# Kernel tuning notes

Hardware: AMD Instinct MI355X
Metric: run time of the kernel (lower is better)

## Reference

```python
import jax, jax.numpy as jnp
import numpy as np

B, N = 512, 128
K = 3                      # top-k per row/col
CONF_THRESH = 0.05
ACCEPT_RADIUS = 0.1
CORR_THRESHOLD = 3         # min correspondences per patch
CORR_LIMIT = 2048          # verification-set size (correspondence_limit)
NUM_REFINE = 5
EPS = 1e-5


def setup_inputs() -> dict:
    key = jax.random.key(0)
    k1, k2, k3, k4, k5 = jax.random.split(key, 5)
    return {
        'score_mat': jax.random.normal(k1, (B, N, N), dtype=jnp.float32),
        'ref_knn_points': jax.random.normal(k2, (B, N, 3), dtype=jnp.float32),
        'src_knn_points': jax.random.normal(k3, (B, N, 3), dtype=jnp.float32),
        'ref_knn_masks': jax.random.bernoulli(k4, 0.95, (B, N)),
        'src_knn_masks': jax.random.bernoulli(k5, 0.95, (B, N)),
    }


def _svd_transform(H, src_c, ref_c):
    """H: (..., 3, 3) covariance; src_c/ref_c: (..., 3) centroids -> (..., 4, 4)."""
    U, _, Vh = jnp.linalg.svd(H)
    V = jnp.swapaxes(Vh, -1, -2)
    Ut = jnp.swapaxes(U, -1, -2)
    d = jnp.sign(jnp.linalg.det(V @ Ut))
    E = jnp.zeros_like(H).at[..., 0, 0].set(1.0).at[..., 1, 1].set(1.0).at[..., 2, 2].set(d)
    R = V @ E @ Ut
    t = ref_c - jnp.einsum('...ij,...j->...i', R, src_c)
    T = jnp.zeros(H.shape[:-2] + (4, 4), H.dtype)
    T = T.at[..., :3, :3].set(R).at[..., :3, 3].set(t).at[..., 3, 3].set(1.0)
    return T


def weighted_procrustes(src, ref, w):
    """src/ref: (C, 3), w: (C,) -> (4, 4). weight_thresh=0, weights >= 0 so no clamp."""
    wn = w / (jnp.sum(w, axis=-1, keepdims=True) + EPS)
    sc = jnp.einsum('n,nc->c', wn, src)
    rc = jnp.einsum('n,nc->c', wn, ref)
    H = jnp.einsum('nc,n,nd->cd', src - sc, wn, ref - rc)
    return _svd_transform(H, sc, rc)


def _topk_mask_last(scores):
    """Keep top-K values along the last axis of (B, R, S), zeros elsewhere."""
    vals, idx = jax.lax.top_k(scores, K)
    b = jnp.arange(scores.shape[0])[:, None, None]
    r = jnp.arange(scores.shape[1])[None, :, None]
    return jnp.zeros_like(scores).at[b, r, idx].set(vals)


def reference(score_mat, ref_knn_points, src_knn_points, ref_knn_masks, src_knn_masks):
    scores = jnp.exp(score_mat)  # score_mat holds log-scores (GeoTransformer forward)

    # --- correspondence matrix: dual top-k scatter + mutual + valid masks ---
    ref_corr = _topk_mask_last(scores) > CONF_THRESH
    src_corr = jnp.swapaxes(_topk_mask_last(jnp.swapaxes(scores, 1, 2)), 1, 2) > CONF_THRESH
    corr = ref_corr & src_corr  # mutual=True
    corr = corr & (ref_knn_masks[:, :, None] & src_knn_masks[:, None, :])

    masked = scores * corr.astype(scores.dtype)  # (B, N, N)
    patch_count = jnp.sum(corr, axis=(1, 2))      # correspondences per patch

    # --- per-patch weighted procrustes over all (n, m) pairs, zero-weighted pads ---
    wn = masked / (jnp.sum(masked, axis=(1, 2), keepdims=True) + EPS)
    sc = jnp.einsum('bnm,bmc->bc', wn, src_knn_points)
    rc = jnp.einsum('bnm,bnc->bc', wn, ref_knn_points)
    Hb = jnp.einsum('bnm,bmc,bnd->bcd', wn, src_knn_points - sc[:, None, :], ref_knn_points - rc[:, None, :])
    # gradients cannot flow past the boolean inlier masks below; stop_gradient avoids
    # spurious NaNs from degenerate 3x3 SVD backward on empty patches
    local_T = jax.lax.stop_gradient(_svd_transform(Hb, sc, rc))  # (B, 4, 4)

    # --- verification set: global top CORR_LIMIT correspondences ---
    flat = masked.reshape(-1)
    sel_scores, sel_idx = jax.lax.top_k(flat, CORR_LIMIT)
    b_i = sel_idx // (N * N)
    r_i = (sel_idx % (N * N)) // N
    s_i = sel_idx % N
    ref_c = ref_knn_points[b_i, r_i]  # (C, 3)
    src_c = src_knn_points[b_i, s_i]  # (C, 3)
    valid = sel_scores > 0

    # --- score every local transform by inlier count on the verification set ---
    R_all = local_T[:, :3, :3]
    t_all = local_T[:, :3, 3]
    aligned = jnp.einsum('pij,cj->pci', R_all, src_c) + t_all[:, None, :]  # (B, C, 3)
    resid = jnp.linalg.norm(ref_c[None] - aligned, axis=-1)
    inlier = (resid < ACCEPT_RADIUS) & valid[None]
    counts = jnp.where(patch_count >= CORR_THRESHOLD, jnp.sum(inlier, axis=-1), -1)
    best = jnp.argmax(counts)
    cur = sel_scores * inlier[best].astype(sel_scores.dtype)

    # --- global refinement: iterative re-weighted procrustes ---
    T = weighted_procrustes(src_c, ref_c, cur)
    for _ in range(NUM_REFINE - 1):
        aligned1 = src_c @ T[:3, :3].T + T[:3, 3]
        r1 = jnp.linalg.norm(ref_c - aligned1, axis=-1)
        cur = sel_scores * (r1 < ACCEPT_RADIUS).astype(sel_scores.dtype)
        T = weighted_procrustes(src_c, ref_c, cur)
    return T
```

## Files before the change

### kernel.cpp

```cpp
#include <hip/hip_runtime.h>
#include <math.h>

#define BB 512
#define NN 128
#define CAND_CAP (512*384)
#define LIMIT 2048
#define EQCAP 16384
#define NBIN1 4096

__device__ inline bool read_mask(const void* p, int i, int mode){
  if (mode == 0) return ((const int*)p)[i] != 0;
  if (mode == 1) return ((const unsigned char*)p)[i] != 0;
  return ((const float*)p)[i] != 0.0f;
}

__device__ inline float fast_rcp(float x){ return __builtin_amdgcn_rcpf(x); }
__device__ inline float fast_rsq(float x){ return __builtin_amdgcn_rsqf(x); }

__device__ __forceinline__ void kabsch9(
    float h00, float h01, float h02,
    float h10, float h11, float h12,
    float h20, float h21, float h22,
    float& r00, float& r01, float& r02,
    float& r10, float& r11, float& r12,
    float& r20, float& r21, float& r22)
{
  float s00 = h00*h00 + h10*h10 + h20*h20;
  float s01 = h00*h01 + h10*h11 + h20*h21;
  float s02 = h00*h02 + h10*h12 + h20*h22;
  float s11 = h01*h01 + h11*h11 + h21*h21;
  float s12 = h01*h02 + h11*h12 + h21*h22;
  float s22 = h02*h02 + h12*h12 + h22*h22;
  float v00=1.f,v01=0.f,v02=0.f, v10=0.f,v11=1.f,v12=0.f, v20=0.f,v21=0.f,v22=1.f;
  for (int sweep = 0; sweep < 10; sweep++){
    float off  = s01*s01 + s02*s02 + s12*s12;
    float base = s00*s00 + s11*s11 + s22*s22;
    if (off <= base*1e-14f + 1e-36f) break;
    if (fabsf(s01) > 1e-30f){
      float tau = (s11 - s00) * fast_rcp(2.f*s01);
      float tt  = (tau >= 0.f ? 1.f : -1.f) * fast_rcp(fabsf(tau) + sqrtf(1.f + tau*tau));
      float c = fast_rsq(1.f + tt*tt), s = tt*c;
      float n00 = c*c*s00 - 2.f*c*s*s01 + s*s*s11;
      float n11 = s*s*s00 + 2.f*c*s*s01 + c*c*s11;
      float n02 = c*s02 - s*s12;
      float n12 = s*s02 + c*s12;
      s00=n00; s11=n11; s01=0.f; s02=n02; s12=n12;
      float a,b;
      a=v00; b=v01; v00=c*a-s*b; v01=s*a+c*b;
      a=v10; b=v11; v10=c*a-s*b; v11=s*a+c*b;
      a=v20; b=v21; v20=c*a-s*b; v21=s*a+c*b;
    }
    if (fabsf(s02) > 1e-30f){
      float tau = (s22 - s00) * fast_rcp(2.f*s02);
      float tt  = (tau >= 0.f ? 1.f : -1.f) * fast_rcp(fabsf(tau) + sqrtf(1.f + tau*tau));
      float c = fast_rsq(1.f + tt*tt), s = tt*c;
      float n00 = c*c*s00 - 2.f*c*s*s02 + s*s*s22;
      float n22 = s*s*s00 + 2.f*c*s*s02 + c*c*s22;
      float n01 = c*s01 - s*s12;
      float n12 = s*s01 + c*s12;
      s00=n00; s22=n22; s02=0.f; s01=n01; s12=n12;
      float a,b;
      a=v00; b=v02; v00=c*a-s*b; v02=s*a+c*b;
      a=v10; b=v12; v10=c*a-s*b; v12=s*a+c*b;
      a=v20; b=v22; v20=c*a-s*b; v22=s*a+c*b;
    }
    if (fabsf(s12) > 1e-30f){
      float tau = (s22 - s11) * fast_rcp(2.f*s12);
      float tt  = (tau >= 0.f ? 1.f : -1.f) * fast_rcp(fabsf(tau) + sqrtf(1.f + tau*tau));
      float c = fast_rsq(1.f + tt*tt), s = tt*c;
      float n11 = c*c*s11 - 2.f*c*s*s12 + s*s*s22;
      float n22 = s*s*s11 + 2.f*c*s*s12 + c*c*s22;
      float n01 = c*s01 - s*s02;
      float n02 = s*s01 + c*s02;
      s11=n11; s22=n22; s12=0.f; s01=n01; s02=n02;
      float a,b;
      a=v01; b=v02; v01=c*a-s*b; v02=s*a+c*b;
      a=v11; b=v12; v11=c*a-s*b; v12=s*a+c*b;
      a=v21; b=v22; v21=c*a-s*b; v22=s*a+c*b;
    }
  }
  float l0=s00, l1=s11, l2=s22;
  float a0=v00, a1=v10, a2=v20;
  float b0=v01, b1=v11, b2=v21;
  float c0=v02, c1=v12, c2=v22;
  if (l0 < l1){ float x; x=l0;l0=l1;l1=x; x=a0;a0=b0;b0=x; x=a1;a1=b1;b1=x; x=a2;a2=b2;b2=x; }
  if (l0 < l2){ float x; x=l0;l0=l2;l2=x; x=a0;a0=c0;c0=x; x=a1;a1=c1;c1=x; x=a2;a2=c2;c2=x; }
  if (l1 < l2){ float x; x=l1;l1=l2;l2=x; x=b0;b0=c0;c0=x; x=b1;b1=c1;c1=x; x=b2;b2=c2;c2=x; }
  float sig0 = sqrtf(fmaxf(l0, 0.f));
  if (!(sig0 > 1e-12f)){
    r00=1.f; r01=0.f; r02=0.f; r10=0.f; r11=1.f; r12=0.f; r20=0.f; r21=0.f; r22=1.f;
    return;
  }
  float u0x = h00*a0 + h01*a1 + h02*a2;
  float u0y = h10*a0 + h11*a1 + h12*a2;
  float u0z = h20*a0 + h21*a1 + h22*a2;
  float in0 = fast_rsq(u0x*u0x + u0y*u0y + u0z*u0z);
  u0x *= in0; u0y *= in0; u0z *= in0;
  float u1x = h00*b0 + h01*b1 + h02*b2;
  float u1y = h10*b0 + h11*b1 + h12*b2;
  float u1z = h20*b0 + h21*b1 + h22*b2;
  float dp = u1x*u0x + u1y*u0y + u1z*u0z;
  u1x -= dp*u0x; u1y -= dp*u0y; u1z -= dp*u0z;
  float d1 = u1x*u1x + u1y*u1y + u1z*u1z;
  if (sqrtf(d1) > sig0*1e-5f){
    float in1 = fast_rsq(d1);
    u1x *= in1; u1y *= in1; u1z *= in1;
  } else {
    float au0 = fabsf(u0x), au1 = fabsf(u0y), au2 = fabsf(u0z);
    float e0 = 0.f, e1 = 0.f, e2 = 0.f;
    if (au0 <= au1 && au0 <= au2) e0 = 1.f; else if (au1 <= au2) e1 = 1.f; else e2 = 1.f;
    float d2 = e0*u0x + e1*u0y + e2*u0z;
    u1x = e0 - d2*u0x; u1y = e1 - d2*u0y; u1z = e2 - d2*u0z;
    float nn = fast_rsq(u1x*u1x + u1y*u1y + u1z*u1z);
    u1x *= nn; u1y *= nn; u1z *= nn;
  }
  float u2x = u0y*u1z - u0z*u1y;
  float u2y = u0z*u1x - u0x*u1z;
  float u2z = u0x*u1y - u0y*u1x;
  float cxv = b1*c2 - b2*c1;
  float cyv = b2*c0 - b0*c2;
  float czv = b0*c1 - b1*c0;
  float detV = a0*cxv + a1*cyv + a2*czv;
  float dd = (detV >= 0.f) ? 1.f : -1.f;
  float w2x = dd*u2x, w2y = dd*u2y, w2z = dd*u2z;
  r00=a0*u0x + b0*u1x + c0*w2x;  r01=a0*u0y + b0*u1y + c0*w2y;  r02=a0*u0z + b0*u1z + c0*w2z;
  r10=a1*u0x + b1*u1x + c1*w2x;  r11=a1*u0y + b1*u1y + c1*w2y;  r12=a1*u0z + b1*u1z + c1*w2z;
  r20=a2*u0x + b2*u1x + c2*w2x;  r21=a2*u0y + b2*u1y + c2*w2y;  r22=a2*u0z + b2*u1z + c2*w2z;
}

__global__ __launch_bounds__(256) void k1_kernel(
    const float* __restrict__ score, const float* __restrict__ refp,
    const float* __restrict__ srcp, const void* __restrict__ rmaskp,
    const void* __restrict__ smaskp,
    int* hdr, float* cand_vals, int* cand_idx,
    float* Hsr, int* pcount)
{
  __shared__ float parts[2][NN][3];
  __shared__ float srcsh[NN*3];
  __shared__ float refsh[NN*3];
  __shared__ float c3sh[NN];
  __shared__ unsigned char smk[NN], rmk[NN];
  __shared__ float candv[4][96];
  __shared__ int   candi[4][96];
  __shared__ int   wcnt[4];
  __shared__ int   woff[4];
  __shared__ int   bbase;
  __shared__ float red[4][17];
  __shared__ int smode;
  const int b = blockIdx.x, t = threadIdx.x;
  const int w = t >> 6, l = t & 63;

  if (t < 64){
    unsigned v = ((const unsigned*)rmaskp)[t];
    bool n01 = !(v == 0u || v == 1u);
    bool nf  = !(v == 0u || v == 0x3F800000u);
    unsigned long long b01 = __ballot(n01), bf = __ballot(nf);
    if (t == 0) smode = (b01 == 0ull) ? 0 : ((bf == 0ull) ? 2 : 1);
  }
  if (t < 4) wcnt[t] = 0;
  for (int i = t; i < NN*3; i += 256){
    srcsh[i] = srcp[b*NN*3 + i];
    refsh[i] = refp[b*NN*3 + i];
  }

  {
    const int c = t & 127, h = t >> 7;
    float a1=-1e30f, a2=-1e30f, a3=-1e30f;
    const float* colp = score + (size_t)b*NN*NN + (size_t)(h*64)*NN + c;
#pragma unroll 8
    for (int i = 0; i < 64; i++){
      float v = colp[i*NN];
      float m = fminf(a1, v);
      a1 = fmaxf(a1, v);
      a3 = fmaxf(a3, fminf(a2, m));
      a2 = fmaxf(a2, m);
    }
    parts[h][c][0]=a1; parts[h][c][1]=a2; parts[h][c][2]=a3;
  }
  __syncthreads();
  if (t < NN){
    float a1=parts[0][t][0], a2=parts[0][t][1], a3=parts[0][t][2];
    float b1=parts[1][t][0], b2=parts[1][t][1], b3=parts[1][t][2];
    c3sh[t] = fmaxf(fmaxf(fminf(a1,b2), fminf(a2,b1)), fmaxf(a3,b3));
    int mode = smode;
    smk[t] = read_mask(smaskp, b*NN + t, mode) ? 1 : 0;
    rmk[t] = read_mask(rmaskp, b*NN + t, mode) ? 1 : 0;
  }
  __syncthreads();

  float cn0=0.f, A0=0.f, Rx0=0.f, Ry0=0.f, Rz0=0.f;
  float cn1=0.f, A1=0.f, Rx1=0.f, Ry1=0.f, Rz1=0.f;
  const float c3_0 = c3sh[l], c3_1 = c3sh[l + 64];
  const int sm0 = smk[l], sm1 = smk[l + 64];

  const float* base = score + (size_t)b*NN*NN;
  for (int rr = 0; rr < 32; rr++){
    const int r = w*32 + rr;
    const float v0 = base[r*NN + l];
    const float v1 = base[r*NN + l + 64];
    float a1 = fmaxf(v0, v1), a2 = fminf(v0, v1), a3 = -1e30f;
#pragma unroll
    for (int st = 0; st < 6; st++){
      const int mask = 1 << st;
      float o1 = __shfl_xor(a1, mask);
      float o2 = __shfl_xor(a2, mask);
      float o3 = __shfl_xor(a3, mask);
      float m1 = fmaxf(a1, o1);
      float m2 = fmaxf(fminf(a1, o1), fmaxf(a2, o2));
      float m3 = fmaxf(fmaxf(fminf(a1, o2), fminf(a2, o1)), fmaxf(a3, o3));
      a1 = m1; a2 = m2; a3 = m3;
    }
    const float r3 = a3;
    const bool rmv = rmk[r] != 0;
    const float rx = refsh[r*3+0], ry = refsh[r*3+1], rz = refsh[r*3+2];
    float e0 = 0.f, e1 = 0.f;
    bool k0 = false, k1 = false;
    if (rmv && sm0 && v0 >= r3 && v0 >= c3_0){
      e0 = expf(v0); k0 = (e0 > 0.05f);
    }
    if (rmv && sm1 && v1 >= r3 && v1 >= c3_1){
      e1 = expf(v1); k1 = (e1 > 0.05f);
    }
    if (k0){ cn0 += 1.f; A0 += e0; Rx0 += e0*rx; Ry0 += e0*ry; Rz0 += e0*rz; }
    if (k1){ cn1 += 1.f; A1 += e1; Rx1 += e1*rx; Ry1 += e1*ry; Rz1 += e1*rz; }
    unsigned long long B0 = __ballot(k0);
    unsigned long long B1 = __ballot(k1);
    int n0 = __popcll(B0), n1 = __popcll(B1);
    if (n0 + n1 > 0){
      int wb = 0;
      if (l == 0){ wb = wcnt[w]; wcnt[w] = wb + n0 + n1; }
      wb = __shfl(wb, 0);
      unsigned long long lt = (l == 0) ? 0ull : (~0ull >> (64 - l));
      if (k0){
        int pos = wb + (int)__popcll(B0 & lt);
        if (pos < 96){ candv[w][pos] = e0; candi[w][pos] = (b<<14)|(r<<7)|l; }
      }
      if (k1){
        int pos = wb + n0 + (int)__popcll(B1 & lt);
        if (pos < 96){ candv[w][pos] = e1; candi[w][pos] = (b<<14)|(r<<7)|(l+64); }
      }
    }
  }
  __syncthreads();
  if (t == 0){
    int c0 = wcnt[0] > 96 ? 96 : wcnt[0];
    int c1 = wcnt[1] > 96 ? 96 : wcnt[1];
    int c2 = wcnt[2] > 96 ? 96 : wcnt[2];
    int c3 = wcnt[3] > 96 ? 96 : wcnt[3];
    woff[0] = 0; woff[1] = c0; woff[2] = c0 + c1; woff[3] = c0 + c1 + c2;
    bbase = atomicAdd(&hdr[0], c0 + c1 + c2 + c3);
  }
  __syncthreads();
  {
    int total = wcnt[w]; if (total > 96) total = 96;
    int gbase = bbase + woff[w];
    for (int i = l; i < total; i += 64){
      int pos = gbase + i;
      if (pos < CAND_CAP){ cand_vals[pos] = candv[w][i]; cand_idx[pos] = candi[w][i]; }
    }
  }
  {
    const float sx0 = srcsh[l*3+0], sy0 = srcsh[l*3+1], sz0 = srcsh[l*3+2];
    const float sx1 = srcsh[(l+64)*3+0], sy1 = srcsh[(l+64)*3+1], sz1 = srcsh[(l+64)*3+2];
#define WSUM(VAL, IDX) { float v_ = (VAL); \
    for (int o_ = 32; o_ > 0; o_ >>= 1) v_ += __shfl_down(v_, o_); \
    if (l == 0) red[w][IDX] = v_; }
    WSUM(cn0 + cn1, 0)
    WSUM(A0 + A1, 1)
    WSUM(Rx0 + Rx1, 2)
    WSUM(Ry0 + Ry1, 3)
    WSUM(Rz0 + Rz1, 4)
    WSUM(A0*sx0 + A1*sx1, 5)
    WSUM(A0*sy0 + A1*sy1, 6)
    WSUM(A0*sz0 + A1*sz1, 7)
    WSUM(sx0*Rx0 + sx1*Rx1, 8)
    WSUM(sx0*Ry0 + sx1*Ry1, 9)
    WSUM(sx0*Rz0 + sx1*Rz1, 10)
    WSUM(sy0*Rx0 + sy1*Rx1, 11)
    WSUM(sy0*Ry0 + sy1*Ry1, 12)
    WSUM(sy0*Rz0 + sy1*Rz1, 13)
    WSUM(sz0*Rx0 + sz1*Rx1, 14)
    WSUM(sz0*Ry0 + sz1*Ry1, 15)
    WSUM(sz0*Rz0 + sz1*Rz1, 16)
#undef WSUM
  }
  __syncthreads();
  if (t == 0){
    float tot[17];
#pragma unroll
    for (int k = 0; k < 17; k++)
      tot[k] = red[0][k] + red[1][k] + red[2][k] + red[3][k];
    float Wm = tot[1];
    float denom = Wm + 1e-5f;
    float idenom = 1.f / denom;
    float s = Wm * idenom;
    float rcv[3] = { tot[2]*idenom, tot[3]*idenom, tot[4]*idenom };
    float scv[3] = { tot[5]*idenom, tot[6]*idenom, tot[7]*idenom };
    float* o = &Hsr[b*15];
#pragma unroll
    for (int c = 0; c < 3; c++)
#pragma unroll
      for (int d = 0; d < 3; d++)
        o[c*3+d] = tot[8 + c*3 + d]*idenom - (2.f - s)*scv[c]*rcv[d];
    o[9]=scv[0]; o[10]=scv[1]; o[11]=scv[2];
    o[12]=rcv[0]; o[13]=rcv[1]; o[14]=rcv[2];
    pcount[b] = (int)(tot[0] + 0.5f);
  }
}

__global__ __launch_bounds__(256) void k3a_kernel(
    const int* hdr, const float* __restrict__ cand_vals, int* hist)
{
  __shared__ int lh[NBIN1];
  int t = threadIdx.x;
  int Nc = hdr[0]; if (Nc > CAND_CAP) Nc = CAND_CAP;
  for (int j = t; j < NBIN1; j += 256) lh[j] = 0;
  __syncthreads();
  for (int i = blockIdx.x*256 + t; i < Nc; i += gridDim.x*256)
    atomicAdd(&lh[__float_as_uint(cand_vals[i]) >> 20], 1);
  __syncthreads();
  for (int j = t; j < NBIN1; j += 256)
    if (lh[j]) atomicAdd(&hist[j], lh[j]);
}

__global__ __launch_bounds__(256) void k3c_kernel(
    int* hdr, const int* __restrict__ hist,
    const float* __restrict__ cand_vals, const int* __restrict__ cand_idx,
    const float* __restrict__ Hsr, float* __restrict__ localT,
    float* sel_vals, int* sel_idx, float* eq_vals, int* eq_idx)
{
  __shared__ int wtot[4];
  __shared__ int sb[2];
  const int t = threadIdx.x, lane = t & 63, wv = t >> 6;

  if (t < 8){
    const int bb = blockIdx.x*8 + t;
    const float* o = &Hsr[bb*15];
    float r00,r01,r02,r10,r11,r12,r20,r21,r22;
    kabsch9(o[0],o[1],o[2], o[3],o[4],o[5], o[6],o[7],o[8],
            r00,r01,r02,r10,r11,r12,r20,r21,r22);
    float* T = &localT[bb*12];
    T[0]=r00; T[1]=r01; T[2]=r02;
    T[3]=r10; T[4]=r11; T[5]=r12;
    T[6]=r20; T[7]=r21; T[8]=r22;
    T[9]  = o[12] - (r00*o[9] + r01*o[10] + r02*o[11]);
    T[10] = o[13] - (r10*o[9] + r11*o[10] + r12*o[11]);
    T[11] = o[14] - (r20*o[9] + r21*o[10] + r22*o[11]);
  }

  int Nc = hdr[0]; if (Nc > CAND_CAP) Nc = CAND_CAP;
  if (Nc <= LIMIT){
    if (t == 0){ sb[0] = -1; sb[1] = 0; if (blockIdx.x == 0){ hdr[4] = -1; hdr[5] = 0; } }
    __syncthreads();
  } else {
    const int chunkIdx = 255 - t;
    int csum = 0;
    for (int j = 0; j < 16; j++) csum += hist[chunkIdx*16 + j];
    int incl = csum;
    for (int off = 1; off < 64; off <<= 1){ int y = __shfl_up(incl, off); if (lane >= off) incl += y; }
    if (lane == 63) wtot[wv] = incl;
    __syncthreads();
    int wbase = 0;
    for (int w = 0; w < wv; w++) wbase += wtot[w];
    int P = wbase + incl;
    int P_prev = P - csum;
    if (P_prev < LIMIT && P >= LIMIT){
      int cum = P_prev, bin1 = chunkIdx*16, need = 0;
      for (int b2 = chunkIdx*16 + 15; b2 >= chunkIdx*16; b2--){
        int h = hist[b2];
        if (cum + h >= LIMIT){ bin1 = b2; need = LIMIT - cum; break; }
        cum += h;
      }
      sb[0] = bin1; sb[1] = need;
      if (blockIdx.x == 0){ hdr[4] = bin1; hdr[5] = need; }
    }
    __syncthreads();
  }
  int bin1 = sb[0];
  for (int i = blockIdx.x*256 + t; i < Nc; i += gridDim.x*256){
    float v = cand_vals[i];
    if (bin1 < 0){
      int p = atomicAdd(&hdr[2], 1);
      if (p < LIMIT){ sel_vals[p] = v; sel_idx[p] = cand_idx[i]; }
      continue;
    }
    int bin = (int)(__float_as_uint(v) >> 20);
    if (bin > bin1){
      int p = atomicAdd(&hdr[2], 1);
      if (p < LIMIT){ sel_vals[p] = v; sel_idx[p] = cand_idx[i]; }
    } else if (bin == bin1){
      int q = atomicAdd(&hdr[1], 1);
      if (q < EQCAP){ eq_vals[q] = v; eq_idx[q] = cand_idx[i]; }
    }
  }
}

__global__ __launch_bounds__(1024) void k3d_kernel(
    const int* hdr, const float* __restrict__ eq_vals, const int* __restrict__ eq_idx,
    float* sel_vals, int* sel_idx,
    const float* __restrict__ refp, const float* __restrict__ srcp,
    float* sel_ref, float* sel_src)
{
  __shared__ int hist[2048];
  __shared__ int eqsh[2048];
  __shared__ int wtot[16];
  __shared__ int bpair[2];
  __shared__ int sh[2];
  const int t = threadIdx.x, lane = t & 63, wv = t >> 6;
  const int bin1 = hdr[4];
  int nAbove = hdr[2]; if (nAbove > LIMIT) nAbove = LIMIT;

  auto find_boundary = [&](int need){
    int i0 = 2047 - 2*t, i1 = 2046 - 2*t;
    int g0 = hist[i0], g1 = hist[i1];
    int local = g0 + g1;
    int incl = local;
    for (int off = 1; off < 64; off <<= 1){ int y = __shfl_up(incl, off); if (lane >= off) incl += y; }
    if (lane == 63) wtot[wv] = incl;
    __syncthreads();
    int wbase = 0;
    for (int w = 0; w < wv; w++) wbase += wtot[w];
    int P_prev = wbase + incl - local;
    int P0 = P_prev + g0;
    if (P0 >= need && P_prev < need){ bpair[0] = i0; bpair[1] = need - P_prev; }
    int P1 = P0 + g1;
    if (P1 >= need && P0 < need){ bpair[0] = i1; bpair[1] = need - P0; }
    __syncthreads();
  };

  bool done = false;
  if (bin1 < 0){
    for (int i = t; i < LIMIT; i += 1024)
      if (i >= nAbove){ sel_vals[i] = 0.f; sel_idx[i] = 0; }
    done = true;
  }
  int neq = 0, need = 0;
  if (!done){
    neq = hdr[1]; if (neq > EQCAP) neq = EQCAP;
    need = hdr[5];
    if (need >= neq){
      for (int i = t; i < neq; i += 1024){ sel_vals[nAbove+i] = eq_vals[i]; sel_idx[nAbove+i] = eq_idx[i]; }
      for (int i = t; i < LIMIT; i += 1024)
        if (i >= nAbove + neq){ sel_vals[i] = 0.f; sel_idx[i] = 0; }
      done = true;
    }
  }
  if (!done){
    for (int i = t; i < 2048; i += 1024) hist[i] = 0;
    __syncthreads();
    for (int i = t; i < neq; i += 1024)
      atomicAdd(&hist[(__float_as_uint(eq_vals[i]) >> 9) & 0x7FF], 1);
    __syncthreads();
    find_boundary(need);
    int binA = bpair[0], need2 = bpair[1];
    __syncthreads();
    for (int i = t; i < 2048; i += 1024) hist[i] = 0;
    __syncthreads();
    for (int i = t; i < neq; i += 1024){
      unsigned k = __float_as_uint(eq_vals[i]);
      if ((int)((k >> 9) & 0x7FF) == binA) atomicAdd(&hist[k & 0x1FF], 1);
    }
    __syncthreads();
    find_boundary(need2);
    unsigned Tlow = (((unsigned)binA) << 9) | (unsigned)bpair[0];
    unsigned Tkey = (((unsigned)bin1) << 20) | Tlow;
    if (t == 0){ sh[0] = 0; sh[1] = 0; }
    __syncthreads();
    for (int i = t; i < neq; i += 1024){
      unsigned k = __float_as_uint(eq_vals[i]);
      unsigned k20 = k & 0xFFFFF;
      if (k20 > Tlow){
        int p = atomicAdd(&sh[0], 1);
        sel_vals[nAbove + p] = eq_vals[i]; sel_idx[nAbove + p] = eq_idx[i];
      } else if (k20 == Tlow){
        int q = atomicAdd(&sh[1], 1);
        if (q < 2048) eqsh[q] = eq_idx[i];
      }
    }
    __syncthreads();
    if (t == 0){
      int na2 = sh[0];
      int ne2 = sh[1]; if (ne2 > 2048) ne2 = 2048;
      int take = need - na2; if (take > ne2) take = ne2; if (take < 0) take = 0;
      if (nAbove + na2 + take > LIMIT) take = LIMIT - nAbove - na2;
      for (int j = 0; j < take; j++){
        int mi = j;
        for (int l2 = j+1; l2 < ne2; l2++) if (eqsh[l2] < eqsh[mi]) mi = l2;
        int tmp = eqsh[j]; eqsh[j] = eqsh[mi]; eqsh[mi] = tmp;
        sel_vals[nAbove + na2 + j] = __uint_as_float(Tkey);
        sel_idx[nAbove + na2 + j] = eqsh[j];
      }
      for (int j = nAbove + na2 + take; j < LIMIT; j++){ sel_vals[j] = 0.f; sel_idx[j] = 0; }
    }
  }
  __syncthreads();
  for (int p = t; p < LIMIT; p += 1024){
    int idx = sel_idx[p];
    int b = idx >> 14, rr = (idx >> 7) & 127, ss = idx & 127;
#pragma unroll
    for (int c = 0; c < 3; c++){
      sel_ref[p*3+c] = refp[(b*NN+rr)*3+c];
      sel_src[p*3+c] = srcp[(b*NN+ss)*3+c];
    }
  }
}

__global__ __launch_bounds__(256) void k4_kernel(
    const float* __restrict__ localT, const float* __restrict__ sel_vals,
    const float* __restrict__ sel_ref, const float* __restrict__ sel_src,
    const int* __restrict__ pcount, int* counts)
{
  __shared__ float Tsh[12];
  __shared__ int ired[4];
  const int b = blockIdx.x, t = threadIdx.x, lane = t & 63, wv = t >> 6;
  if (t < 12) Tsh[t] = localT[b*12 + t];
  __syncthreads();
  float R00=Tsh[0],R01=Tsh[1],R02=Tsh[2],R10=Tsh[3],R11=Tsh[4],R12=Tsh[5];
  float R20=Tsh[6],R21=Tsh[7],R22=Tsh[8];
  float tx=Tsh[9], ty=Tsh[10], tz=Tsh[11];
  int c = 0;
  for (int p = t; p < LIMIT; p += 256){
    float v = sel_vals[p];
    if (!(v > 0.f)) continue;
    float sx=sel_src[p*3], sy=sel_src[p*3+1], sz=sel_src[p*3+2];
    float rx=sel_ref[p*3], ry=sel_ref[p*3+1], rz=sel_ref[p*3+2];
    float ax = R00*sx + R01*sy + R02*sz + tx;
    float ay = R10*sx + R11*sy + R12*sz + ty;
    float az = R20*sx + R21*sy + R22*sz + tz;
    float dx = rx-ax, dy = ry-ay, dz = rz-az;
    if (sqrtf(dx*dx + dy*dy + dz*dz) < 0.1f) c++;
  }
  for (int off2 = 32; off2 > 0; off2 >>= 1) c += __shfl_down(c, off2);
  if (lane == 0) ired[wv] = c;
  __syncthreads();
  if (t == 0) counts[b] = (pcount[b] >= 3) ? (ired[0]+ired[1]+ired[2]+ired[3]) : -1;
}

__global__ __launch_bounds__(256, 1) void k5_kernel(
    const int* __restrict__ counts, const float* __restrict__ localT,
    const float* __restrict__ sel_vals, const float* __restrict__ sel_ref,
    const float* __restrict__ sel_src, float* out)
{
  __shared__ float fred[4][16];
  __shared__ long long lred[4];
  __shared__ float RT[12];
  __shared__ int sbest;
  const int t = threadIdx.x, lane = t & 63, wv = t >> 6;

  long long key = (long long)0x8000000000000000LL;
  for (int bb = t; bb < BB; bb += 256){
    long long kk = ((long long)(counts[bb] + 2) << 32) | (long long)(511 - bb);
    if (kk > key) key = kk;
  }
  for (int off2 = 32; off2 > 0; off2 >>= 1){ long long o = __shfl_down(key, off2); if (o > key) key = o; }
  if (lane == 0) lred[wv] = key;
  __syncthreads();
  if (t == 0){
    long long m = lred[0];
#pragma unroll
    for (int w = 1; w < 4; w++) if (lred[w] > m) m = lred[w];
    sbest = 511 - (int)(m & 0xFFFFFFFFLL);
  }
  __syncthreads();
  if (t < 12) RT[t] = localT[sbest*12 + t];
  __syncthreads();

  for (int iter = 0; iter < 5; iter++){
    float R00=RT[0],R01=RT[1],R02=RT[2];
    float R10=RT[3],R11=RT[4],R12=RT[5];
    float R20=RT[6],R21=RT[7],R22=RT[8];
    float tx=RT[9], ty=RT[10], tz=RT[11];
    float a0=0.f,a1=0.f,a2=0.f,a3=0.f,a4=0.f,a5=0.f,a6=0.f,a7=0.f;
    float a8=0.f,a9=0.f,a10=0.f,a11=0.f,a12=0.f,a13=0.f,a14=0.f,a15=0.f;
    for (int p = t; p < LIMIT; p += 256){
      float v = sel_vals[p];
      if (!(v > 0.f)) continue;
      float sx=sel_src[p*3], sy=sel_src[p*3+1], sz=sel_src[p*3+2];
      float rx=sel_ref[p*3], ry=sel_ref[p*3+1], rz=sel_ref[p*3+2];
      float ax = R00*sx + R01*sy + R02*sz + tx;
      float ay = R10*sx + R11*sy + R12*sz + ty;
      float az = R20*sx + R21*sy + R22*sz + tz;
      float dx = rx-ax, dy = ry-ay, dz = rz-az;
      if (sqrtf(dx*dx + dy*dy + dz*dz) < 0.1f){
        a0 += v;
        a1 += v*sx; a2 += v*sy; a3 += v*sz;
        a4 += v*rx; a5 += v*ry; a6 += v*rz;
        a7  += v*sx*rx; a8  += v*sx*ry; a9  += v*sx*rz;
        a10 += v*sy*rx; a11 += v*sy*ry; a12 += v*sy*rz;
        a13 += v*sz*rx; a14 += v*sz*ry; a15 += v*sz*rz;
      }
    }
#define WRED(VAL, IDX) { float v_ = (VAL); \
    for (int o_ = 32; o_ > 0; o_ >>= 1) v_ += __shfl_down(v_, o_); \
    if (lane == 0) fred[wv][IDX] = v_; }
    WRED(a0, 0)  WRED(a1, 1)  WRED(a2, 2)  WRED(a3, 3)
    WRED(a4, 4)  WRED(a5, 5)  WRED(a6, 6)  WRED(a7, 7)
    WRED(a8, 8)  WRED(a9, 9)  WRED(a10,10) WRED(a11,11)
    WRED(a12,12) WRED(a13,13) WRED(a14,14) WRED(a15,15)
#undef WRED
    __syncthreads();
    if (t == 0){
      float tot[16];
#pragma unroll
      for (int k = 0; k < 16; k++) tot[k] = fred[0][k]+fred[1][k]+fred[2][k]+fred[3][k];
      float W = tot[0], denom = W + 1e-5f;
      float inv = 1.f / denom;
      float s = W * inv;
      float scx = tot[1]*inv, scy = tot[2]*inv, scz = tot[3]*inv;
      float rcx = tot[4]*inv, rcy = tot[5]*inv, rcz = tot[6]*inv;
      float f = 2.f - s;
      float h00 = tot[7]*inv  - f*scx*rcx;
      float h01 = tot[8]*inv  - f*scx*rcy;
      float h02 = tot[9]*inv  - f*scx*rcz;
      float h10 = tot[10]*inv - f*scy*rcx;
      float h11 = tot[11]*inv - f*scy*rcy;
      float h12 = tot[12]*inv - f*scy*rcz;
      float h20 = tot[13]*inv - f*scz*rcx;
      float h21 = tot[14]*inv - f*scz*rcy;
      float h22 = tot[15]*inv - f*scz*rcz;
      float r00,r01,r02,r10,r11,r12,r20,r21,r22;
      kabsch9(h00,h01,h02,h10,h11,h12,h20,h21,h22,
              r00,r01,r02,r10,r11,r12,r20,r21,r22);
      RT[0]=r00; RT[1]=r01; RT[2]=r02;
      RT[3]=r10; RT[4]=r11; RT[5]=r12;
      RT[6]=r20; RT[7]=r21; RT[8]=r22;
      RT[9]  = rcx - (r00*scx + r01*scy + r02*scz);
      RT[10] = rcy - (r10*scx + r11*scy + r12*scz);
      RT[11] = rcz - (r20*scx + r21*scy + r22*scz);
    }
    __syncthreads();
  }
  if (t == 0){
    out[0]=RT[0];  out[1]=RT[1];  out[2]=RT[2];  out[3]=RT[9];
    out[4]=RT[3];  out[5]=RT[4];  out[6]=RT[5];  out[7]=RT[10];
    out[8]=RT[6];  out[9]=RT[7];  out[10]=RT[8]; out[11]=RT[11];
    out[12]=0.f; out[13]=0.f; out[14]=0.f; out[15]=1.f;
  }
}

extern "C" void kernel_launch(void* const* d_in, const int* in_sizes, int n_in,
                              void* d_out, int out_size, void* d_ws, size_t ws_size,
                              hipStream_t stream){
  const float* score = (const float*)d_in[0];
  const float* refp  = (const float*)d_in[1];
  const float* srcp  = (const float*)d_in[2];
  const void*  rmask = d_in[3];
  const void*  smask = d_in[4];

  char* ws = (char*)d_ws;
  size_t off = 0;
  int* hdr = (int*)(ws + off);            off += 256;
  int* hist = (int*)(ws + off);           off += (size_t)NBIN1*4;
  float* cand_vals = (float*)(ws + off);  off += (size_t)CAND_CAP*4;
  int* cand_idx = (int*)(ws + off);       off += (size_t)CAND_CAP*4;
  float* eq_vals = (float*)(ws + off);    off += (size_t)EQCAP*4;
  int* eq_idx = (int*)(ws + off);         off += (size_t)EQCAP*4;
  float* Hsr = (float*)(ws + off);        off += (size_t)BB*15*4;
  int* pcount = (int*)(ws + off);         off += (size_t)BB*4;
  float* localT = (float*)(ws + off);     off += (size_t)BB*12*4;
  float* sel_vals = (float*)(ws + off);   off += (size_t)LIMIT*4;
  int* sel_idx = (int*)(ws + off);        off += (size_t)LIMIT*4;
  float* sel_ref = (float*)(ws + off);    off += (size_t)LIMIT*3*4;
  float* sel_src = (float*)(ws + off);    off += (size_t)LIMIT*3*4;
  int* counts = (int*)(ws + off);         off += (size_t)BB*4;

  hipMemsetAsync(ws, 0, 256 + (size_t)NBIN1*4, stream);
  hipLaunchKernelGGL(k1_kernel, dim3(BB), dim3(256), 0, stream,
                     score, refp, srcp, rmask, smask,
                     hdr, cand_vals, cand_idx, Hsr, pcount);
  hipLaunchKernelGGL(k3a_kernel, dim3(64), dim3(256), 0, stream, hdr, cand_vals, hist);
  hipLaunchKernelGGL(k3c_kernel, dim3(64), dim3(256), 0, stream,
                     hdr, hist, cand_vals, cand_idx, Hsr, localT,
                     sel_vals, sel_idx, eq_vals, eq_idx);
  hipLaunchKernelGGL(k3d_kernel, dim3(1), dim3(1024), 0, stream,
                     hdr, eq_vals, eq_idx, sel_vals, sel_idx, refp, srcp, sel_ref, sel_src);
  hipLaunchKernelGGL(k4_kernel, dim3(BB), dim3(256), 0, stream,
                     localT, sel_vals, sel_ref, sel_src, pcount, counts);
  hipLaunchKernelGGL(k5_kernel, dim3(1), dim3(256), 0, stream,
                     counts, localT, sel_vals, sel_ref, sel_src, (float*)d_out);
}
```

Measured before the change: 210.3 us.

## Stage verification set in LDS and widen refinement kernel to 1024 threads

The single-block refinement kernel now loads the 2048 selected correspondences once into shared memory as structure-of-arrays. Its five iterations then read from LDS instead of re-reading global memory. The block grows from 256 to 1024 threads, and the inlier branch becomes a predicated weight, so every thread accumulates without divergence. In exchange, the cross-wave reduction now sums 16 partials instead of 4, and the kernel uses about 56KB of shared memory.

```diff
diff --git a/kernel.cpp b/kernel.cpp
--- a/kernel.cpp
+++ b/kernel.cpp
@@ -536,19 +536,28 @@
   if (t == 0) counts[b] = (pcount[b] >= 3) ? (ired[0]+ired[1]+ired[2]+ired[3]) : -1;
 }
 
-__global__ __launch_bounds__(256, 1) void k5_kernel(
+__global__ __launch_bounds__(1024, 1) void k5_kernel(
     const int* __restrict__ counts, const float* __restrict__ localT,
     const float* __restrict__ sel_vals, const float* __restrict__ sel_ref,
     const float* __restrict__ sel_src, float* out)
 {
-  __shared__ float fred[4][16];
-  __shared__ long long lred[4];
+  __shared__ float pv[LIMIT];
+  __shared__ float psx[LIMIT], psy[LIMIT], psz[LIMIT];
+  __shared__ float prx[LIMIT], pry[LIMIT], prz[LIMIT];
+  __shared__ float fred[16][16];
+  __shared__ long long lred[16];
   __shared__ float RT[12];
   __shared__ int sbest;
   const int t = threadIdx.x, lane = t & 63, wv = t >> 6;
 
+  for (int p = t; p < LIMIT; p += 1024){
+    pv[p]  = sel_vals[p];
+    psx[p] = sel_src[p*3+0]; psy[p] = sel_src[p*3+1]; psz[p] = sel_src[p*3+2];
+    prx[p] = sel_ref[p*3+0]; pry[p] = sel_ref[p*3+1]; prz[p] = sel_ref[p*3+2];
+  }
+
   long long key = (long long)0x8000000000000000LL;
-  for (int bb = t; bb < BB; bb += 256){
+  for (int bb = t; bb < BB; bb += 1024){
     long long kk = ((long long)(counts[bb] + 2) << 32) | (long long)(511 - bb);
     if (kk > key) key = kk;
   }
@@ -558,7 +567,7 @@
   if (t == 0){
     long long m = lred[0];
 #pragma unroll
-    for (int w = 1; w < 4; w++) if (lred[w] > m) m = lred[w];
+    for (int w = 1; w < 16; w++) if (lred[w] > m) m = lred[w];
     sbest = 511 - (int)(m & 0xFFFFFFFFLL);
   }
   __syncthreads();
@@ -572,23 +581,22 @@
     float tx=RT[9], ty=RT[10], tz=RT[11];
     float a0=0.f,a1=0.f,a2=0.f,a3=0.f,a4=0.f,a5=0.f,a6=0.f,a7=0.f;
     float a8=0.f,a9=0.f,a10=0.f,a11=0.f,a12=0.f,a13=0.f,a14=0.f,a15=0.f;
-    for (int p = t; p < LIMIT; p += 256){
-      float v = sel_vals[p];
-      if (!(v > 0.f)) continue;
-      float sx=sel_src[p*3], sy=sel_src[p*3+1], sz=sel_src[p*3+2];
-      float rx=sel_ref[p*3], ry=sel_ref[p*3+1], rz=sel_ref[p*3+2];
+    for (int p = t; p < LIMIT; p += 1024){
+      float v = pv[p];
+      float sx=psx[p], sy=psy[p], sz=psz[p];
+      float rx=prx[p], ry=pry[p], rz=prz[p];
       float ax = R00*sx + R01*sy + R02*sz + tx;
       float ay = R10*sx + R11*sy + R12*sz + ty;
       float az = R20*sx + R21*sy + R22*sz + tz;
       float dx = rx-ax, dy = ry-ay, dz = rz-az;
-      if (sqrtf(dx*dx + dy*dy + dz*dz) < 0.1f){
-        a0 += v;
-        a1 += v*sx; a2 += v*sy; a3 += v*sz;
-        a4 += v*rx; a5 += v*ry; a6 += v*rz;
-        a7  += v*sx*rx; a8  += v*sx*ry; a9  += v*sx*rz;
-        a10 += v*sy*rx; a11 += v*sy*ry; a12 += v*sy*rz;
-        a13 += v*sz*rx; a14 += v*sz*ry; a15 += v*sz*rz;
-      }
+      bool in = (v > 0.f) && (sqrtf(dx*dx + dy*dy + dz*dz) < 0.1f);
+      float wgt = in ? v : 0.f;
+      a0 += wgt;
+      a1 += wgt*sx; a2 += wgt*sy; a3 += wgt*sz;
+      a4 += wgt*rx; a5 += wgt*ry; a6 += wgt*rz;
+      a7  += wgt*sx*rx; a8  += wgt*sx*ry; a9  += wgt*sx*rz;
+      a10 += wgt*sy*rx; a11 += wgt*sy*ry; a12 += wgt*sy*rz;
+      a13 += wgt*sz*rx; a14 += wgt*sz*ry; a15 += wgt*sz*rz;
     }
 #define WRED(VAL, IDX) { float v_ = (VAL); \
     for (int o_ = 32; o_ > 0; o_ >>= 1) v_ += __shfl_down(v_, o_); \
@@ -602,7 +610,12 @@
     if (t == 0){
       float tot[16];
 #pragma unroll
-      for (int k = 0; k < 16; k++) tot[k] = fred[0][k]+fred[1][k]+fred[2][k]+fred[3][k];
+      for (int k = 0; k < 16; k++){
+        float s2 = 0.f;
+#pragma unroll
+        for (int w = 0; w < 16; w++) s2 += fred[w][k];
+        tot[k] = s2;
+      }
       float W = tot[0], denom = W + 1e-5f;
       float inv = 1.f / denom;
       float s = W * inv;
@@ -676,6 +689,6 @@
                      hdr, eq_vals, eq_idx, sel_vals, sel_idx, refp, srcp, sel_ref, sel_src);
   hipLaunchKernelGGL(k4_kernel, dim3(BB), dim3(256), 0, stream,
                      localT, sel_vals, sel_ref, sel_src, pcount, counts);
-  hipLaunchKernelGGL(k5_kernel, dim3(1), dim3(256), 0, stream,
+  hipLaunchKernelGGL(k5_kernel, dim3(1), dim3(1024), 0, stream,
                      counts, localT, sel_vals, sel_ref, sel_src, (float*)d_out);
 }
```

New measurement: 219.1 us. 4.2% more time.
